# Kernel tuning notes

Hardware: AMD Instinct MI355X
Metric: run time of the kernel (lower is better)

## Reference

```python
import jax, jax.numpy as jnp
import numpy as np

B, N, D = 16, 4096, 128          # graphs, points per graph, feature dim
RATIO = 0.25
M = int(N * RATIO)               # 1024 sampled points per graph (static)
RADIUS = 0.2


def setup_inputs() -> dict:
    key = jax.random.key(0)
    k1, k2 = jax.random.split(key)
    x = jax.random.normal(k1, (B * N, D), dtype=jnp.float32)
    pos = jax.random.uniform(k2, (B * N, 3), dtype=jnp.float32)  # unit cube
    batch = jnp.repeat(jnp.arange(B, dtype=jnp.int32), N)        # sorted, equal-size graphs
    return {"x": x, "pos": pos, "batch": batch}


def _fps(pos_g):
    """Farthest point sampling on one graph. pos_g: [N,3] -> [M] int indices.
    Deterministic start at index 0 (random_start=False, i.e. eval mode)."""
    def step(carry, _):
        dist, last = carry
        d = jnp.sum((pos_g - pos_g[last]) ** 2, axis=-1)   # [N]
        dist = jnp.minimum(dist, d)                        # dist to nearest selected
        nxt = jnp.argmax(dist).astype(jnp.int32)
        return (dist, nxt), last
    init = (jnp.full((pos_g.shape[0],), jnp.inf, pos_g.dtype), jnp.int32(0))
    _, idx = jax.lax.scan(step, init, None, length=M)
    return idx  # [M]


def reference(x, pos, batch):
    # Equal-size graphs -> reshape instead of segment bookkeeping.
    pos_b = pos.reshape(B, N, 3)
    x_b = x.reshape(B, N, D)

    # FPS per graph, vmapped (sequential greedy selection inside lax.scan).
    idx = jax.vmap(_fps)(pos_b)                                    # [B, M]

    sampled_pos = jnp.take_along_axis(pos_b, idx[:, :, None], axis=1)  # [B, M, 3]
    sampled_x = jnp.take_along_axis(x_b, idx[:, :, None], axis=1)      # [B, M, D]

    # radius_graph within each graph: boolean adjacency (j within r of i, no self loops).
    diff = sampled_pos[:, :, None, :] - sampled_pos[:, None, :, :]     # [B, M, M, 3]
    d2 = jnp.sum(diff * diff, axis=-1)                                 # [B, M, M]
    adj = (d2 <= RADIUS * RADIUS) & ~jnp.eye(M, dtype=bool)[None]      # [B, M, M]

    sampled_batch = jnp.repeat(jnp.arange(B, dtype=batch.dtype), M)    # [B*M]
    return (sampled_x.reshape(B * M, D),
            sampled_pos.reshape(B * M, 3),
            sampled_batch,
            adj)
```

## Files before the change

### kernel.cpp

```cpp
#include <hip/hip_runtime.h>
#include <stdint.h>

#define BB 16
#define NN 4096
#define DD 128
#define MM 1024
#define RADIUS2 0.04f
#define TPB 256
#define PPT 16
#define NPAIR (PPT / 2)
#define NW  (TPB / 64)

typedef unsigned long long u64;
typedef unsigned int u32;
typedef float f32x2 __attribute__((ext_vector_type(2)));
typedef unsigned int uint2v __attribute__((ext_vector_type(2)));

__device__ __forceinline__ u32 umin2(u32 a, u32 b) { return a < b ? a : b; }
__device__ __forceinline__ u32 umin3(u32 a, u32 b, u32 c) { return umin2(umin2(a, b), c); }
__device__ __forceinline__ float fmax3(float a, float b, float c) { return fmaxf(fmaxf(a, b), c); }

template <int CTRL>
__device__ __forceinline__ float dpp_fmax(float v) {
    int o = __builtin_amdgcn_update_dpp(0, __float_as_int(v), CTRL, 0xF, 0xF, true);
    return fmaxf(v, __int_as_float(o));
}
template <int CTRL>
__device__ __forceinline__ u32 dpp_umin(u32 v) {
    u32 o = (u32)__builtin_amdgcn_update_dpp(0, (int)v, CTRL, 0xF, 0xF, true);
    return umin2(v, o);
}

__device__ __forceinline__ float xor16_fmax(float v) {
#if __has_builtin(__builtin_amdgcn_permlane16_swap)
    uint2v r = __builtin_amdgcn_permlane16_swap(__float_as_uint(v), __float_as_uint(v), false, false);
    return fmaxf(__uint_as_float(r[0]), __uint_as_float(r[1]));
#else
    int o = __builtin_amdgcn_ds_swizzle(__float_as_int(v), 0x401F);
    return fmaxf(v, __int_as_float(o));
#endif
}
__device__ __forceinline__ u32 xor16_umin(u32 v) {
#if __has_builtin(__builtin_amdgcn_permlane16_swap)
    uint2v r = __builtin_amdgcn_permlane16_swap(v, v, false, false);
    return umin2(r[0], r[1]);
#else
    u32 o = (u32)__builtin_amdgcn_ds_swizzle((int)v, 0x401F);
    return umin2(v, o);
#endif
}
__device__ __forceinline__ float xor32_fmax(float v) {
#if __has_builtin(__builtin_amdgcn_permlane32_swap)
    uint2v r = __builtin_amdgcn_permlane32_swap(__float_as_uint(v), __float_as_uint(v), false, false);
    return fmaxf(__uint_as_float(r[0]), __uint_as_float(r[1]));
#else
    return fmaxf(v, __shfl_xor(v, 32, 64));
#endif
}
__device__ __forceinline__ u32 xor32_umin(u32 v) {
#if __has_builtin(__builtin_amdgcn_permlane32_swap)
    uint2v r = __builtin_amdgcn_permlane32_swap(v, v, false, false);
    return umin2(r[0], r[1]);
#else
    return umin2(v, __shfl_xor(v, 32, 64));
#endif
}

__device__ __forceinline__ float wave_fmax(float v) {
    v = dpp_fmax<0xB1>(v);
    v = dpp_fmax<0x4E>(v);
    v = dpp_fmax<0x141>(v);
    v = dpp_fmax<0x140>(v);
    v = xor16_fmax(v);
    v = xor32_fmax(v);
    return v;
}
__device__ __forceinline__ u32 wave_umin(u32 v) {
    v = dpp_umin<0xB1>(v);
    v = dpp_umin<0x4E>(v);
    v = dpp_umin<0x141>(v);
    v = dpp_umin<0x140>(v);
    v = xor16_umin(v);
    v = xor32_umin(v);
    return v;
}

__global__ __launch_bounds__(TPB) void fps_kernel(const float* __restrict__ pos,
                                                  int* __restrict__ idx_out) {
    const int b   = blockIdx.x;
    const int tid = threadIdx.x;
    const int wid = tid >> 6;

    __shared__ float4 pos4[NN];
    __shared__ float4 fpart[2][NW];
    __shared__ u32    ipart[2][NW];

    const float* pg = pos + (size_t)b * NN * 3;
    for (int k = tid; k < NN * 3; k += TPB)
        ((float*)&pos4[k / 3])[k % 3] = pg[k];
    __syncthreads();

    f32x2 px[NPAIR], py[NPAIR], pz[NPAIR], dist2[NPAIR];
#pragma unroll
    for (int j = 0; j < NPAIR; ++j) {
        float4 a = pos4[tid * PPT + 2 * j];
        float4 c = pos4[tid * PPT + 2 * j + 1];
        px[j] = (f32x2){a.x, c.x};
        py[j] = (f32x2){a.y, c.y};
        pz[j] = (f32x2){a.z, c.z};
        dist2[j] = (f32x2){__builtin_inff(), __builtin_inff()};
    }

    if (tid == 0) idx_out[b * MM] = 0;
    float4 lp = pos4[0];
    float lx = lp.x, ly = lp.y, lz = lp.z;

    for (int m = 1; m < MM; ++m) {
        {
#pragma clang fp contract(off)
            f32x2 vx = {lx, lx}, vy = {ly, ly}, vz = {lz, lz};
#pragma unroll
            for (int j = 0; j < NPAIR; ++j) {
                f32x2 dx = px[j] - vx;
                f32x2 dy = py[j] - vy;
                f32x2 dz = pz[j] - vz;
                f32x2 d  = dx * dx + dy * dy;
                d = d + dz * dz;
                dist2[j] = __builtin_elementwise_min(dist2[j], d);
            }
        }

        float t0 = fmaxf(dist2[0].x, dist2[0].y);
        float t1 = fmaxf(dist2[1].x, dist2[1].y);
        float t2 = fmaxf(dist2[2].x, dist2[2].y);
        float t3 = fmaxf(dist2[3].x, dist2[3].y);
        float t4 = fmaxf(dist2[4].x, dist2[4].y);
        float t5 = fmaxf(dist2[5].x, dist2[5].y);
        float t6 = fmaxf(dist2[6].x, dist2[6].y);
        float t7 = fmaxf(dist2[7].x, dist2[7].y);
        float tmax = fmax3(fmax3(t0, t1, t2), fmax3(t3, t4, t5), fmaxf(t6, t7));

        u32 c[PPT];
#pragma unroll
        for (int j = 0; j < NPAIR; ++j) {
            c[2 * j]     = (dist2[j].x == tmax) ? (u32)(2 * j)     : 64u;
            c[2 * j + 1] = (dist2[j].y == tmax) ? (u32)(2 * j + 1) : 64u;
        }
        u32 a0 = umin3(c[0],  c[1],  c[2]);
        u32 a1 = umin3(c[3],  c[4],  c[5]);
        u32 a2 = umin3(c[6],  c[7],  c[8]);
        u32 a3 = umin3(c[9],  c[10], c[11]);
        u32 a4 = umin3(c[12], c[13], c[14]);
        u32 sl = umin3(umin3(a0, a1, a2), umin2(a3, a4), c[15]);
        u32 gidx = (u32)(tid * PPT) + sl;

        float4 sp = pos4[gidx];

        float wmax = wave_fmax(tmax);
        u32 cand = (tmax == wmax) ? gidx : 0xFFFFFFFFu;
        u32 widx = wave_umin(cand);

        const int buf = m & 1;
        if (cand == widx) {
            fpart[buf][wid] = make_float4(wmax, sp.x, sp.y, sp.z);
            ipart[buf][wid] = widx;
        }
        __syncthreads();

        float4 q0 = fpart[buf][0];
        float4 q1 = fpart[buf][1];
        float4 q2 = fpart[buf][2];
        float4 q3 = fpart[buf][3];
        float g = fmaxf(fmaxf(q0.x, q1.x), fmaxf(q2.x, q3.x));
        float nx = q3.y, ny = q3.z, nz = q3.w;
        bool b2 = (q2.x == g); nx = b2 ? q2.y : nx; ny = b2 ? q2.z : ny; nz = b2 ? q2.w : nz;
        bool b1 = (q1.x == g); nx = b1 ? q1.y : nx; ny = b1 ? q1.z : ny; nz = b1 ? q1.w : nz;
        bool b0 = (q0.x == g); nx = b0 ? q0.y : nx; ny = b0 ? q0.z : ny; nz = b0 ? q0.w : nz;
        lx = nx; ly = ny; lz = nz;

        if (tid == 0) {
            u32 li = ipart[buf][3];
            li = b2 ? ipart[buf][2] : li;
            li = b1 ? ipart[buf][1] : li;
            li = b0 ? ipart[buf][0] : li;
            idx_out[b * MM + m] = (int)li;
        }
    }
}

__global__ void gather_x_kernel(const float* __restrict__ x,
                                const int* __restrict__ idx,
                                float* __restrict__ out) {
    int t = blockIdx.x * blockDim.x + threadIdx.x;
    if (t >= BB * MM * DD / 4) return;
    int row = t >> 5;
    int c4  = (t & 31) << 2;
    int b   = row >> 10;
    int n   = idx[row];
    const float4 v = *(const float4*)(x + ((size_t)(b * NN + n) * DD + c4));
    *(float4*)(out + (size_t)row * DD + c4) = v;
}

__global__ void gather_pb_kernel(const float* __restrict__ pos,
                                 const int* __restrict__ idx,
                                 float* __restrict__ spos,
                                 float* __restrict__ sbatch) {
    int r = blockIdx.x * blockDim.x + threadIdx.x;
    if (r >= BB * MM) return;
    int b = r >> 10;
    int n = idx[r];
    const float* p = pos + (size_t)(b * NN + n) * 3;
    spos[r * 3 + 0] = p[0];
    spos[r * 3 + 1] = p[1];
    spos[r * 3 + 2] = p[2];
    sbatch[r] = (float)b;
}

__global__ void adj_kernel(const float* __restrict__ spos,
                           float* __restrict__ adj) {
    int row = blockIdx.x;
    int b   = row >> 10;
    int i   = row & (MM - 1);
    const float* pb = spos + (size_t)b * MM * 3;
    float xi = pb[i * 3 + 0];
    float yi = pb[i * 3 + 1];
    float zi = pb[i * 3 + 2];

    int j0 = threadIdx.x << 2;
    float4 r;
    float* o = adj + (size_t)row * MM;
#pragma unroll
    for (int k = 0; k < 4; ++k) {
        int j = j0 + k;
        float dx = xi - pb[j * 3 + 0];
        float dy = yi - pb[j * 3 + 1];
        float dz = zi - pb[j * 3 + 2];
        float d2 = __fadd_rn(__fadd_rn(__fmul_rn(dx, dx), __fmul_rn(dy, dy)),
                             __fmul_rn(dz, dz));
        float v = (d2 <= RADIUS2 && j != i) ? 1.0f : 0.0f;
        ((float*)&r)[k] = v;
    }
    *(float4*)(o + j0) = r;
}

extern "C" void kernel_launch(void* const* d_in, const int* in_sizes, int n_in,
                              void* d_out, int out_size, void* d_ws, size_t ws_size,
                              hipStream_t stream) {
    const float* x   = (const float*)d_in[0];
    const float* pos = (const float*)d_in[1];

    float* out    = (float*)d_out;
    int*   idx_ws = (int*)d_ws;

    float* sx   = out;
    float* spos = sx + (size_t)BB * MM * DD;
    float* sbat = spos + (size_t)BB * MM * 3;
    float* adj  = sbat + (size_t)BB * MM;

    fps_kernel<<<BB, TPB, 0, stream>>>(pos, idx_ws);
    gather_x_kernel<<<(BB * MM * DD / 4 + 255) / 256, 256, 0, stream>>>(x, idx_ws, sx);
    gather_pb_kernel<<<(BB * MM + 255) / 256, 256, 0, stream>>>(pos, idx_ws, spos, sbat);
    adj_kernel<<<BB * MM, 256, 0, stream>>>(spos, adj);
}
```

Measured before the change: 718.7 us.

## Run FPS with a single wavefront per graph, removing block barriers

The FPS kernel moves from four wavefronts per graph (16 points per thread) to a single 64-lane wavefront (64 points per thread). The per-iteration shared-memory partial exchange and __syncthreads are replaced by wave reductions plus readfirstlane/readlane broadcasts of the winner's coordinates. This removes barrier and LDS round-trip latency on the serial 1023-step critical path. In exchange each lane does four times as much distance and argmax work per step, and only 16 wavefronts run in total, so ALU throughput per step may become the limit.

```diff
diff --git a/kernel.cpp b/kernel.cpp
--- a/kernel.cpp
+++ b/kernel.cpp
@@ -6,10 +6,9 @@
 #define DD 128
 #define MM 1024
 #define RADIUS2 0.04f
-#define TPB 256
-#define PPT 16
+#define TPB 64
+#define PPT 64
 #define NPAIR (PPT / 2)
-#define NW  (TPB / 64)
 
 typedef unsigned long long u64;
 typedef unsigned int u32;
@@ -18,7 +17,6 @@
 
 __device__ __forceinline__ u32 umin2(u32 a, u32 b) { return a < b ? a : b; }
 __device__ __forceinline__ u32 umin3(u32 a, u32 b, u32 c) { return umin2(umin2(a, b), c); }
-__device__ __forceinline__ float fmax3(float a, float b, float c) { return fmaxf(fmaxf(a, b), c); }
 
 template <int CTRL>
 __device__ __forceinline__ float dpp_fmax(float v) {
@@ -30,7 +28,6 @@
     u32 o = (u32)__builtin_amdgcn_update_dpp(0, (int)v, CTRL, 0xF, 0xF, true);
     return umin2(v, o);
 }
-
 __device__ __forceinline__ float xor16_fmax(float v) {
 #if __has_builtin(__builtin_amdgcn_permlane16_swap)
     uint2v r = __builtin_amdgcn_permlane16_swap(__float_as_uint(v), __float_as_uint(v), false, false);
@@ -65,7 +62,6 @@
     return umin2(v, __shfl_xor(v, 32, 64));
 #endif
 }
-
 __device__ __forceinline__ float wave_fmax(float v) {
     v = dpp_fmax<0xB1>(v);
     v = dpp_fmax<0x4E>(v);
@@ -87,31 +83,29 @@
 
 __global__ __launch_bounds__(TPB) void fps_kernel(const float* __restrict__ pos,
                                                   int* __restrict__ idx_out) {
-    const int b   = blockIdx.x;
-    const int tid = threadIdx.x;
-    const int wid = tid >> 6;
+    const int b    = blockIdx.x;
+    const int lane = threadIdx.x;
 
     __shared__ float4 pos4[NN];
-    __shared__ float4 fpart[2][NW];
-    __shared__ u32    ipart[2][NW];
 
     const float* pg = pos + (size_t)b * NN * 3;
-    for (int k = tid; k < NN * 3; k += TPB)
+    for (int k = lane; k < NN * 3; k += TPB)
         ((float*)&pos4[k / 3])[k % 3] = pg[k];
     __syncthreads();
 
+    const int base = lane * PPT;
     f32x2 px[NPAIR], py[NPAIR], pz[NPAIR], dist2[NPAIR];
 #pragma unroll
     for (int j = 0; j < NPAIR; ++j) {
-        float4 a = pos4[tid * PPT + 2 * j];
-        float4 c = pos4[tid * PPT + 2 * j + 1];
+        float4 a = pos4[base + 2 * j];
+        float4 c = pos4[base + 2 * j + 1];
         px[j] = (f32x2){a.x, c.x};
         py[j] = (f32x2){a.y, c.y};
         pz[j] = (f32x2){a.z, c.z};
         dist2[j] = (f32x2){__builtin_inff(), __builtin_inff()};
     }
 
-    if (tid == 0) idx_out[b * MM] = 0;
+    if (lane == 0) idx_out[b * MM] = 0;
     float4 lp = pos4[0];
     float lx = lp.x, ly = lp.y, lz = lp.z;
 
@@ -130,29 +124,33 @@
             }
         }
 
-        float t0 = fmaxf(dist2[0].x, dist2[0].y);
-        float t1 = fmaxf(dist2[1].x, dist2[1].y);
-        float t2 = fmaxf(dist2[2].x, dist2[2].y);
-        float t3 = fmaxf(dist2[3].x, dist2[3].y);
-        float t4 = fmaxf(dist2[4].x, dist2[4].y);
-        float t5 = fmaxf(dist2[5].x, dist2[5].y);
-        float t6 = fmaxf(dist2[6].x, dist2[6].y);
-        float t7 = fmaxf(dist2[7].x, dist2[7].y);
-        float tmax = fmax3(fmax3(t0, t1, t2), fmax3(t3, t4, t5), fmaxf(t6, t7));
-
-        u32 c[PPT];
-#pragma unroll
-        for (int j = 0; j < NPAIR; ++j) {
-            c[2 * j]     = (dist2[j].x == tmax) ? (u32)(2 * j)     : 64u;
-            c[2 * j + 1] = (dist2[j].y == tmax) ? (u32)(2 * j + 1) : 64u;
+        float ta = fmaxf(dist2[0].x, dist2[0].y);
+        float tb = fmaxf(dist2[1].x, dist2[1].y);
+        float tc = fmaxf(dist2[2].x, dist2[2].y);
+        float td = fmaxf(dist2[3].x, dist2[3].y);
+#pragma unroll
+        for (int j = 4; j < NPAIR; j += 4) {
+            ta = fmaxf(ta, fmaxf(dist2[j].x,     dist2[j].y));
+            tb = fmaxf(tb, fmaxf(dist2[j + 1].x, dist2[j + 1].y));
+            tc = fmaxf(tc, fmaxf(dist2[j + 2].x, dist2[j + 2].y));
+            td = fmaxf(td, fmaxf(dist2[j + 3].x, dist2[j + 3].y));
         }
-        u32 a0 = umin3(c[0],  c[1],  c[2]);
-        u32 a1 = umin3(c[3],  c[4],  c[5]);
-        u32 a2 = umin3(c[6],  c[7],  c[8]);
-        u32 a3 = umin3(c[9],  c[10], c[11]);
-        u32 a4 = umin3(c[12], c[13], c[14]);
-        u32 sl = umin3(umin3(a0, a1, a2), umin2(a3, a4), c[15]);
-        u32 gidx = (u32)(tid * PPT) + sl;
+        float tmax = fmaxf(fmaxf(ta, tb), fmaxf(tc, td));
+
+        u32 sa = 64u, sb = 64u, sc = 64u, sd = 64u;
+#pragma unroll
+        for (int j = 0; j < NPAIR; j += 4) {
+            sa = umin3(sa, (dist2[j].x     == tmax) ? (u32)(2 * j)     : 64u,
+                           (dist2[j].y     == tmax) ? (u32)(2 * j + 1) : 64u);
+            sb = umin3(sb, (dist2[j + 1].x == tmax) ? (u32)(2 * j + 2) : 64u,
+                           (dist2[j + 1].y == tmax) ? (u32)(2 * j + 3) : 64u);
+            sc = umin3(sc, (dist2[j + 2].x == tmax) ? (u32)(2 * j + 4) : 64u,
+                           (dist2[j + 2].y == tmax) ? (u32)(2 * j + 5) : 64u);
+            sd = umin3(sd, (dist2[j + 3].x == tmax) ? (u32)(2 * j + 6) : 64u,
+                           (dist2[j + 3].y == tmax) ? (u32)(2 * j + 7) : 64u);
+        }
+        u32 sl = umin3(umin2(sa, sb), sc, sd);
+        u32 gidx = (u32)base + sl;
 
         float4 sp = pos4[gidx];
 
@@ -160,31 +158,12 @@
         u32 cand = (tmax == wmax) ? gidx : 0xFFFFFFFFu;
         u32 widx = wave_umin(cand);
 
-        const int buf = m & 1;
-        if (cand == widx) {
-            fpart[buf][wid] = make_float4(wmax, sp.x, sp.y, sp.z);
-            ipart[buf][wid] = widx;
-        }
-        __syncthreads();
-
-        float4 q0 = fpart[buf][0];
-        float4 q1 = fpart[buf][1];
-        float4 q2 = fpart[buf][2];
-        float4 q3 = fpart[buf][3];
-        float g = fmaxf(fmaxf(q0.x, q1.x), fmaxf(q2.x, q3.x));
-        float nx = q3.y, ny = q3.z, nz = q3.w;
-        bool b2 = (q2.x == g); nx = b2 ? q2.y : nx; ny = b2 ? q2.z : ny; nz = b2 ? q2.w : nz;
-        bool b1 = (q1.x == g); nx = b1 ? q1.y : nx; ny = b1 ? q1.z : ny; nz = b1 ? q1.w : nz;
-        bool b0 = (q0.x == g); nx = b0 ? q0.y : nx; ny = b0 ? q0.z : ny; nz = b0 ? q0.w : nz;
-        lx = nx; ly = ny; lz = nz;
-
-        if (tid == 0) {
-            u32 li = ipart[buf][3];
-            li = b2 ? ipart[buf][2] : li;
-            li = b1 ? ipart[buf][1] : li;
-            li = b0 ? ipart[buf][0] : li;
-            idx_out[b * MM + m] = (int)li;
-        }
+        int owner = (int)(__builtin_amdgcn_readfirstlane((int)widx) >> 6);
+        lx = __int_as_float(__builtin_amdgcn_readlane(__float_as_int(sp.x), owner));
+        ly = __int_as_float(__builtin_amdgcn_readlane(__float_as_int(sp.y), owner));
+        lz = __int_as_float(__builtin_amdgcn_readlane(__float_as_int(sp.z), owner));
+
+        if (lane == 0) idx_out[b * MM + m] = (int)widx;
     }
 }
 
```

New measurement: 1.590 ms. +121.2%, slower.

## Pack two graphs per FPS block and use ballot for argmax owner

Applied to the files above, without the earlier changes.

FPS now runs two graphs per 512-thread block (8 blocks instead of 16), with each half holding its own points in shared memory. The second wave-wide umin reduction is replaced by a ballot plus count-trailing-zeros to pick the owning lane, and indices are buffered in shared memory and written out at the end. Both halves now share every __syncthreads, so each graph waits on the slower one. Halving the block count leaves more CUs idle, so latency per iteration may not improve. The ballot tie-break picks the lowest lane rather than the smallest index, which gives the same result because each lane holds a contiguous range of points.

```diff
diff --git a/kernel.cpp b/kernel.cpp
--- a/kernel.cpp
+++ b/kernel.cpp
@@ -6,10 +6,9 @@
 #define DD 128
 #define MM 1024
 #define RADIUS2 0.04f
-#define TPB 256
+#define TPB 512
 #define PPT 16
 #define NPAIR (PPT / 2)
-#define NW  (TPB / 64)
 
 typedef unsigned long long u64;
 typedef unsigned int u32;
@@ -25,12 +24,6 @@
     int o = __builtin_amdgcn_update_dpp(0, __float_as_int(v), CTRL, 0xF, 0xF, true);
     return fmaxf(v, __int_as_float(o));
 }
-template <int CTRL>
-__device__ __forceinline__ u32 dpp_umin(u32 v) {
-    u32 o = (u32)__builtin_amdgcn_update_dpp(0, (int)v, CTRL, 0xF, 0xF, true);
-    return umin2(v, o);
-}
-
 __device__ __forceinline__ float xor16_fmax(float v) {
 #if __has_builtin(__builtin_amdgcn_permlane16_swap)
     uint2v r = __builtin_amdgcn_permlane16_swap(__float_as_uint(v), __float_as_uint(v), false, false);
@@ -40,15 +33,6 @@
     return fmaxf(v, __int_as_float(o));
 #endif
 }
-__device__ __forceinline__ u32 xor16_umin(u32 v) {
-#if __has_builtin(__builtin_amdgcn_permlane16_swap)
-    uint2v r = __builtin_amdgcn_permlane16_swap(v, v, false, false);
-    return umin2(r[0], r[1]);
-#else
-    u32 o = (u32)__builtin_amdgcn_ds_swizzle((int)v, 0x401F);
-    return umin2(v, o);
-#endif
-}
 __device__ __forceinline__ float xor32_fmax(float v) {
 #if __has_builtin(__builtin_amdgcn_permlane32_swap)
     uint2v r = __builtin_amdgcn_permlane32_swap(__float_as_uint(v), __float_as_uint(v), false, false);
@@ -57,15 +41,6 @@
     return fmaxf(v, __shfl_xor(v, 32, 64));
 #endif
 }
-__device__ __forceinline__ u32 xor32_umin(u32 v) {
-#if __has_builtin(__builtin_amdgcn_permlane32_swap)
-    uint2v r = __builtin_amdgcn_permlane32_swap(v, v, false, false);
-    return umin2(r[0], r[1]);
-#else
-    return umin2(v, __shfl_xor(v, 32, 64));
-#endif
-}
-
 __device__ __forceinline__ float wave_fmax(float v) {
     v = dpp_fmax<0xB1>(v);
     v = dpp_fmax<0x4E>(v);
@@ -75,44 +50,43 @@
     v = xor32_fmax(v);
     return v;
 }
-__device__ __forceinline__ u32 wave_umin(u32 v) {
-    v = dpp_umin<0xB1>(v);
-    v = dpp_umin<0x4E>(v);
-    v = dpp_umin<0x141>(v);
-    v = dpp_umin<0x140>(v);
-    v = xor16_umin(v);
-    v = xor32_umin(v);
-    return v;
-}
 
 __global__ __launch_bounds__(TPB) void fps_kernel(const float* __restrict__ pos,
                                                   int* __restrict__ idx_out) {
-    const int b   = blockIdx.x;
-    const int tid = threadIdx.x;
-    const int wid = tid >> 6;
-
-    __shared__ float4 pos4[NN];
-    __shared__ float4 fpart[2][NW];
-    __shared__ u32    ipart[2][NW];
-
-    const float* pg = pos + (size_t)b * NN * 3;
-    for (int k = tid; k < NN * 3; k += TPB)
-        ((float*)&pos4[k / 3])[k % 3] = pg[k];
+    const int blk  = blockIdx.x;
+    const int tid  = threadIdx.x;
+    const int half = tid >> 8;
+    const int ht   = tid & 255;
+    const int wid  = ht >> 6;
+    const int lane = tid & 63;
+    const int g    = blk * 2 + half;
+
+    __shared__ float4 pos4[2 * NN];
+    __shared__ float4 fpart[2][2][4];
+    __shared__ u32    ipart[2][2][4];
+    __shared__ int    trace[2][MM];
+
+    const float* pg = pos + (size_t)g * NN * 3;
+    float* pbase = (float*)&pos4[half * NN];
+    for (int k = ht; k < NN * 3; k += 256)
+        pbase[(k / 3) * 4 + (k % 3)] = pg[k];
+    if (ht == 0) trace[half][0] = 0;
     __syncthreads();
 
+    const int base = ht * PPT;
+    const float4* mypos = &pos4[half * NN];
     f32x2 px[NPAIR], py[NPAIR], pz[NPAIR], dist2[NPAIR];
 #pragma unroll
     for (int j = 0; j < NPAIR; ++j) {
-        float4 a = pos4[tid * PPT + 2 * j];
-        float4 c = pos4[tid * PPT + 2 * j + 1];
+        float4 a = mypos[base + 2 * j];
+        float4 c = mypos[base + 2 * j + 1];
         px[j] = (f32x2){a.x, c.x};
         py[j] = (f32x2){a.y, c.y};
         pz[j] = (f32x2){a.z, c.z};
         dist2[j] = (f32x2){__builtin_inff(), __builtin_inff()};
     }
 
-    if (tid == 0) idx_out[b * MM] = 0;
-    float4 lp = pos4[0];
+    float4 lp = mypos[0];
     float lx = lp.x, ly = lp.y, lz = lp.z;
 
     for (int m = 1; m < MM; ++m) {
@@ -152,40 +126,45 @@
         u32 a3 = umin3(c[9],  c[10], c[11]);
         u32 a4 = umin3(c[12], c[13], c[14]);
         u32 sl = umin3(umin3(a0, a1, a2), umin2(a3, a4), c[15]);
-        u32 gidx = (u32)(tid * PPT) + sl;
-
-        float4 sp = pos4[gidx];
+        u32 gidx = (u32)base + sl;
+
+        float4 sp = mypos[gidx];
 
         float wmax = wave_fmax(tmax);
-        u32 cand = (tmax == wmax) ? gidx : 0xFFFFFFFFu;
-        u32 widx = wave_umin(cand);
+
+        u64 mk   = __ballot(tmax == wmax);
+        int owner = (int)__builtin_ctzll(mk);
 
         const int buf = m & 1;
-        if (cand == widx) {
-            fpart[buf][wid] = make_float4(wmax, sp.x, sp.y, sp.z);
-            ipart[buf][wid] = widx;
+        if (lane == owner) {
+            fpart[half][buf][wid] = make_float4(wmax, sp.x, sp.y, sp.z);
+            ipart[half][buf][wid] = gidx;
         }
         __syncthreads();
 
-        float4 q0 = fpart[buf][0];
-        float4 q1 = fpart[buf][1];
-        float4 q2 = fpart[buf][2];
-        float4 q3 = fpart[buf][3];
-        float g = fmaxf(fmaxf(q0.x, q1.x), fmaxf(q2.x, q3.x));
+        float4 q0 = fpart[half][buf][0];
+        float4 q1 = fpart[half][buf][1];
+        float4 q2 = fpart[half][buf][2];
+        float4 q3 = fpart[half][buf][3];
+        float gmx = fmaxf(fmaxf(q0.x, q1.x), fmaxf(q2.x, q3.x));
         float nx = q3.y, ny = q3.z, nz = q3.w;
-        bool b2 = (q2.x == g); nx = b2 ? q2.y : nx; ny = b2 ? q2.z : ny; nz = b2 ? q2.w : nz;
-        bool b1 = (q1.x == g); nx = b1 ? q1.y : nx; ny = b1 ? q1.z : ny; nz = b1 ? q1.w : nz;
-        bool b0 = (q0.x == g); nx = b0 ? q0.y : nx; ny = b0 ? q0.z : ny; nz = b0 ? q0.w : nz;
+        bool b2 = (q2.x == gmx); nx = b2 ? q2.y : nx; ny = b2 ? q2.z : ny; nz = b2 ? q2.w : nz;
+        bool b1 = (q1.x == gmx); nx = b1 ? q1.y : nx; ny = b1 ? q1.z : ny; nz = b1 ? q1.w : nz;
+        bool b0 = (q0.x == gmx); nx = b0 ? q0.y : nx; ny = b0 ? q0.z : ny; nz = b0 ? q0.w : nz;
         lx = nx; ly = ny; lz = nz;
 
-        if (tid == 0) {
-            u32 li = ipart[buf][3];
-            li = b2 ? ipart[buf][2] : li;
-            li = b1 ? ipart[buf][1] : li;
-            li = b0 ? ipart[buf][0] : li;
-            idx_out[b * MM + m] = (int)li;
+        if (ht == 0) {
+            u32 li = ipart[half][buf][3];
+            li = b2 ? ipart[half][buf][2] : li;
+            li = b1 ? ipart[half][buf][1] : li;
+            li = b0 ? ipart[half][buf][0] : li;
+            trace[half][m] = (int)li;
         }
     }
+
+    __syncthreads();
+    for (int k = ht; k < MM; k += 256)
+        idx_out[g * MM + k] = trace[half][k];
 }
 
 __global__ void gather_x_kernel(const float* __restrict__ x,
@@ -257,7 +236,7 @@
     float* sbat = spos + (size_t)BB * MM * 3;
     float* adj  = sbat + (size_t)BB * MM;
 
-    fps_kernel<<<BB, TPB, 0, stream>>>(pos, idx_ws);
+    fps_kernel<<<BB / 2, TPB, 0, stream>>>(pos, idx_ws);
     gather_x_kernel<<<(BB * MM * DD / 4 + 255) / 256, 256, 0, stream>>>(x, idx_ws, sx);
     gather_pb_kernel<<<(BB * MM + 255) / 256, 256, 0, stream>>>(pos, idx_ws, spos, sbat);
     adj_kernel<<<BB * MM, 256, 0, stream>>>(spos, adj);
```

After: 1.011 ms. +40.6%, slower.
